# Kernel tuning notes

Hardware: AMD Instinct MI355X
Metric: run time of the kernel (lower is better)

## Reference

```python
import jax, jax.numpy as jnp
import numpy as np

IOU_THRESHOLD = 0.5


def setup_inputs() -> dict:
    key = jax.random.key(0)
    k_xy, k_wh, k_jit, k_cls, k_lab = jax.random.split(key, 5)
    B, P, T, C = 16, 16384, 128, 80
    # valid x1y1x2y2 ground-truth boxes in [0,1]
    xy = jax.random.uniform(k_xy, (B, T, 2), dtype=jnp.float32) * 0.7
    wh = jax.random.uniform(k_wh, (B, T, 2), dtype=jnp.float32) * 0.25 + 0.05
    true_bboxes = jnp.concatenate([xy, xy + wh], axis=-1)  # [B,T,4]
    # predictions: tiled GT boxes + small jitter so many pairs exceed IoU 0.5
    reps = P // T
    base = jnp.tile(true_bboxes, (1, reps, 1))  # [B,P,4]
    pred_bboxes = base + 0.02 * jax.random.normal(k_jit, (B, P, 4), dtype=jnp.float32)
    pred_classes = jax.random.normal(k_cls, (B, P, C), dtype=jnp.float32)
    true_labels = jax.random.randint(k_lab, (B, T), 0, C, dtype=jnp.int64)
    return {
        "pred_bboxes": pred_bboxes,
        "pred_classes": pred_classes,
        "true_bboxes": true_bboxes,
        "true_labels": true_labels,
    }


def _iou_matrix(pred, true):
    # pred [B,P,4], true [B,T,4] -> [B,P,T]
    p = pred[:, :, None, :]  # [B,P,1,4]
    t = true[:, None, :, :]  # [B,1,T,4]
    x1 = jnp.maximum(p[..., 0], t[..., 0])
    y1 = jnp.maximum(p[..., 1], t[..., 1])
    x2 = jnp.minimum(p[..., 2], t[..., 2])
    y2 = jnp.minimum(p[..., 3], t[..., 3])
    inter = jnp.clip(x2 - x1, 0.0) * jnp.clip(y2 - y1, 0.0)
    pa = (pred[..., 2] - pred[..., 0]) * (pred[..., 3] - pred[..., 1])  # [B,P]
    ta = (true[..., 2] - true[..., 0]) * (true[..., 3] - true[..., 1])  # [B,T]
    union = pa[:, :, None] + ta[:, None, :] - inter
    return inter / union


def _smooth_l1(d):
    ad = jnp.abs(d)
    return jnp.where(ad < 1.0, 0.5 * d * d, ad - 0.5)


def reference(pred_bboxes, pred_classes, true_bboxes, true_labels):
    B, P, _ = pred_bboxes.shape
    iou = _iou_matrix(pred_bboxes, true_bboxes)          # [B,P,T]
    max_iou = jnp.max(iou, axis=2)                       # [B,P]
    max_idx = jnp.argmax(iou, axis=2)                    # [B,P]
    matched_true = jnp.take_along_axis(
        true_bboxes, jnp.broadcast_to(max_idx[:, :, None], (B, P, 4)), axis=1
    )                                                    # [B,P,4]
    mask = (max_iou > IOU_THRESHOLD).astype(pred_bboxes.dtype)  # [B,P]
    elem = _smooth_l1(pred_bboxes - matched_true)        # [B,P,4]
    n_matched = jnp.sum(mask)
    bbox_loss = jnp.sum(elem * mask[:, :, None]) / jnp.maximum(4.0 * n_matched, 1.0)
    # classification: per image, first prediction's logits vs first GT label
    logits = pred_classes[:, 0, :]                       # [B,C]
    labels = true_labels[:, 0]                           # [B]
    logp = jax.nn.log_softmax(logits, axis=-1)
    cls_loss = -jnp.mean(jnp.take_along_axis(logp, labels[:, None], axis=1))
    return bbox_loss + cls_loss
```

## Files before the change

kernel.cpp:

```cpp
#include <hip/hip_runtime.h>
#include <hip/hip_bf16.h>
#include <math.h>

#define B_ 16
#define P_ 16384
#define T_ 128
#define C_ 80
#define IOU_THR 0.5f

__device__ __forceinline__ float smooth_l1(float d) {
    float ad = fabsf(d);
    return (ad < 1.0f) ? 0.5f * d * d : ad - 0.5f;
}

__global__ __launch_bounds__(256) void det_loss_main(
        const float* __restrict__ pred_bboxes,
        const float* __restrict__ true_bboxes,
        float* __restrict__ ws)
{
    const int blocks_per_b = P_ / 256;
    const int b    = blockIdx.x / blocks_per_b;
    const int pblk = blockIdx.x % blocks_per_b;
    const int tid  = threadIdx.x;

    __shared__ float4 tb[T_];
    if (tid < T_) {
        tb[tid] = ((const float4*)true_bboxes)[b * T_ + tid];
    }
    __syncthreads();

    const int p = pblk * 256 + tid;
    const float4 pb = ((const float4*)pred_bboxes)[(size_t)b * P_ + p];
    const float pa = (pb.z - pb.x) * (pb.w - pb.y);

    float best = -1.0f;
    int   bidx = 0;
    #pragma unroll 4
    for (int t = 0; t < T_; ++t) {
        const float4 t4 = tb[t];
        const float x1 = fmaxf(pb.x, t4.x);
        const float y1 = fmaxf(pb.y, t4.y);
        const float x2 = fminf(pb.z, t4.z);
        const float y2 = fminf(pb.w, t4.w);
        const float iw = fmaxf(x2 - x1, 0.0f);
        const float ih = fmaxf(y2 - y1, 0.0f);
        const float inter = iw * ih;
        const float ta = (t4.z - t4.x) * (t4.w - t4.y);
        const float iou = inter / (pa + ta - inter);
        if (iou > best) { best = iou; bidx = t; }
    }

    float contrib = 0.0f, cnt = 0.0f;
    if (best > IOU_THR) {
        const float4 t4 = tb[bidx];
        contrib = smooth_l1(pb.x - t4.x) + smooth_l1(pb.y - t4.y)
                + smooth_l1(pb.z - t4.z) + smooth_l1(pb.w - t4.w);
        cnt = 1.0f;
    }

    #pragma unroll
    for (int off = 32; off > 0; off >>= 1) {
        contrib += __shfl_down(contrib, off, 64);
        cnt     += __shfl_down(cnt,     off, 64);
    }
    __shared__ float sc[4], sn[4];
    const int wave = tid >> 6, lane = tid & 63;
    if (lane == 0) { sc[wave] = contrib; sn[wave] = cnt; }
    __syncthreads();
    if (tid == 0) {
        atomicAdd(&ws[0], sc[0] + sc[1] + sc[2] + sc[3]);
        atomicAdd(&ws[1], sn[0] + sn[1] + sn[2] + sn[3]);
    }
}

__global__ __launch_bounds__(64) void det_loss_final(
        const float* __restrict__ pred_classes,
        const int*   __restrict__ true_labels,
        const float* __restrict__ ws,
        float* __restrict__ out)
{
    const int tid = threadIdx.x;
    __shared__ float rowloss[B_];
    if (tid < B_) {
        const float* row = pred_classes + (size_t)tid * P_ * C_;
        const int lab = true_labels[tid * T_];
        float m = -INFINITY;
        for (int c = 0; c < C_; ++c) m = fmaxf(m, row[c]);
        float s = 0.0f;
        for (int c = 0; c < C_; ++c) s += expf(row[c] - m);
        rowloss[tid] = -(row[lab] - m - logf(s));
    }
    __syncthreads();
    if (tid == 0) {
        float cl = 0.0f;
        for (int b = 0; b < B_; ++b) cl += rowloss[b];
        cl *= (1.0f / B_);
        const float bbox = ws[0] / fmaxf(4.0f * ws[1], 1.0f);
        out[0] = bbox + cl;
    }
}

extern "C" void kernel_launch(void* const* d_in, const int* in_sizes, int n_in,
                              void* d_out, int out_size, void* d_ws, size_t ws_size,
                              hipStream_t stream) {
    const float* pred_bboxes  = (const float*)d_in[0];
    const float* pred_classes = (const float*)d_in[1];
    const float* true_bboxes  = (const float*)d_in[2];
    const int*   true_labels  = (const int*)d_in[3];
    float* out = (float*)d_out;
    float* ws  = (float*)d_ws;

    hipMemsetAsync(ws, 0, 2 * sizeof(float), stream);

    det_loss_main<<<B_ * (P_ / 256), 256, 0, stream>>>(pred_bboxes, true_bboxes, ws);
    det_loss_final<<<1, 64, 0, stream>>>(pred_classes, true_labels, ws, out);
}
```

Measured before the change: 158.2 us.

## Process two predictions per thread, use division-free IoU argmax, drop atomics and memset

Each thread now handles two prediction boxes, so every shared-memory load of a ground-truth box is reused twice. The IoU comparison is done by cross-multiplying intersection and union instead of dividing, and the threshold becomes 2*inter > union. Per-block partial sums go to a workspace array, which removes the atomics and the memset launch. The final kernel reduces those partials and computes log-softmax with wave shuffles. The cross-multiplied comparison can pick a different argmax from the reference when values tie or sit near rounding limits.

```diff
diff --git a/kernel.cpp b/kernel.cpp
--- a/kernel.cpp
+++ b/kernel.cpp
@@ -6,7 +6,7 @@
 #define P_ 16384
 #define T_ 128
 #define C_ 80
-#define IOU_THR 0.5f
+
 
 __device__ __forceinline__ float smooth_l1(float d) {
     float ad = fabsf(d);
@@ -18,44 +18,63 @@
         const float* __restrict__ true_bboxes,
         float* __restrict__ ws)
 {
-    const int blocks_per_b = P_ / 256;
+    const int blocks_per_b = P_ / 512;
     const int b    = blockIdx.x / blocks_per_b;
     const int pblk = blockIdx.x % blocks_per_b;
     const int tid  = threadIdx.x;
 
     __shared__ float4 tb[T_];
-    if (tid < T_) {
-        tb[tid] = ((const float4*)true_bboxes)[b * T_ + tid];
-    }
+    if (tid < T_) tb[tid] = ((const float4*)true_bboxes)[b * T_ + tid];
     __syncthreads();
 
-    const int p = pblk * 256 + tid;
-    const float4 pb = ((const float4*)pred_bboxes)[(size_t)b * P_ + p];
-    const float pa = (pb.z - pb.x) * (pb.w - pb.y);
+    const float4* pbase = (const float4*)pred_bboxes + (size_t)b * P_ + pblk * 512;
+    const float4 pA = pbase[tid];
+    const float4 pB = pbase[tid + 256];
+    const float paA = (pA.z - pA.x) * (pA.w - pA.y);
+    const float paB = (pB.z - pB.x) * (pB.w - pB.y);
 
-    float best = -1.0f;
-    int   bidx = 0;
-    #pragma unroll 4
+    float biA = 0.0f, buA = 1.0f; int bxA = 0;
+    float biB = 0.0f, buB = 1.0f; int bxB = 0;
+
+    #pragma unroll 8
     for (int t = 0; t < T_; ++t) {
         const float4 t4 = tb[t];
-        const float x1 = fmaxf(pb.x, t4.x);
-        const float y1 = fmaxf(pb.y, t4.y);
-        const float x2 = fminf(pb.z, t4.z);
-        const float y2 = fminf(pb.w, t4.w);
-        const float iw = fmaxf(x2 - x1, 0.0f);
-        const float ih = fmaxf(y2 - y1, 0.0f);
-        const float inter = iw * ih;
         const float ta = (t4.z - t4.x) * (t4.w - t4.y);
-        const float iou = inter / (pa + ta - inter);
-        if (iou > best) { best = iou; bidx = t; }
+
+        {
+            const float iw = fmaxf(fminf(pA.z, t4.z) - fmaxf(pA.x, t4.x), 0.0f);
+            const float ih = fmaxf(fminf(pA.w, t4.w) - fmaxf(pA.y, t4.y), 0.0f);
+            const float inter = iw * ih;
+            const float u = (paA + ta) - inter;
+            const bool upd = inter * buA > biA * u;
+            biA = upd ? inter : biA;
+            buA = upd ? u : buA;
+            bxA = upd ? t : bxA;
+        }
+        {
+            const float iw = fmaxf(fminf(pB.z, t4.z) - fmaxf(pB.x, t4.x), 0.0f);
+            const float ih = fmaxf(fminf(pB.w, t4.w) - fmaxf(pB.y, t4.y), 0.0f);
+            const float inter = iw * ih;
+            const float u = (paB + ta) - inter;
+            const bool upd = inter * buB > biB * u;
+            biB = upd ? inter : biB;
+            buB = upd ? u : buB;
+            bxB = upd ? t : bxB;
+        }
     }
 
     float contrib = 0.0f, cnt = 0.0f;
-    if (best > IOU_THR) {
-        const float4 t4 = tb[bidx];
-        contrib = smooth_l1(pb.x - t4.x) + smooth_l1(pb.y - t4.y)
-                + smooth_l1(pb.z - t4.z) + smooth_l1(pb.w - t4.w);
-        cnt = 1.0f;
+    if (2.0f * biA > buA) {
+        const float4 m4 = tb[bxA];
+        contrib += smooth_l1(pA.x - m4.x) + smooth_l1(pA.y - m4.y)
+                 + smooth_l1(pA.z - m4.z) + smooth_l1(pA.w - m4.w);
+        cnt += 1.0f;
+    }
+    if (2.0f * biB > buB) {
+        const float4 m4 = tb[bxB];
+        contrib += smooth_l1(pB.x - m4.x) + smooth_l1(pB.y - m4.y)
+                 + smooth_l1(pB.z - m4.z) + smooth_l1(pB.w - m4.w);
+        cnt += 1.0f;
     }
 
     #pragma unroll
@@ -68,35 +87,57 @@
     if (lane == 0) { sc[wave] = contrib; sn[wave] = cnt; }
     __syncthreads();
     if (tid == 0) {
-        atomicAdd(&ws[0], sc[0] + sc[1] + sc[2] + sc[3]);
-        atomicAdd(&ws[1], sn[0] + sn[1] + sn[2] + sn[3]);
+        ws[blockIdx.x]       = sc[0] + sc[1] + sc[2] + sc[3];
+        ws[512 + blockIdx.x] = sn[0] + sn[1] + sn[2] + sn[3];
     }
 }
 
-__global__ __launch_bounds__(64) void det_loss_final(
+__global__ __launch_bounds__(1024) void det_loss_final(
         const float* __restrict__ pred_classes,
         const int*   __restrict__ true_labels,
         const float* __restrict__ ws,
         float* __restrict__ out)
 {
     const int tid = threadIdx.x;
+    const int wave = tid >> 6, lane = tid & 63;
+
     __shared__ float rowloss[B_];
-    if (tid < B_) {
-        const float* row = pred_classes + (size_t)tid * P_ * C_;
-        const int lab = true_labels[tid * T_];
-        float m = -INFINITY;
-        for (int c = 0; c < C_; ++c) m = fmaxf(m, row[c]);
-        float s = 0.0f;
-        for (int c = 0; c < C_; ++c) s += expf(row[c] - m);
-        rowloss[tid] = -(row[lab] - m - logf(s));
+    __shared__ float wc[16], wn[16];
+
+    const float* row = pred_classes + (size_t)wave * P_ * C_;
+    const float v0 = row[lane];
+    const float v1 = (lane < C_ - 64) ? row[lane + 64] : -INFINITY;
+    float m = fmaxf(v0, v1);
+    #pragma unroll
+    for (int off = 32; off > 0; off >>= 1) m = fmaxf(m, __shfl_xor(m, off, 64));
+    float s = expf(v0 - m) + ((lane < C_ - 64) ? expf(v1 - m) : 0.0f);
+    #pragma unroll
+    for (int off = 32; off > 0; off >>= 1) s += __shfl_xor(s, off, 64);
+    if (lane == 0) {
+        const int lab = true_labels[wave * T_];
+        rowloss[wave] = -(row[lab] - m - logf(s));
     }
+
+    float sc = 0.0f, sn = 0.0f;
+    if (tid < 128) {
+        const float4 c4 = ((const float4*)ws)[tid];
+        const float4 n4 = ((const float4*)(ws + 512))[tid];
+        sc = c4.x + c4.y + c4.z + c4.w;
+        sn = n4.x + n4.y + n4.z + n4.w;
+    }
+    #pragma unroll
+    for (int off = 32; off > 0; off >>= 1) {
+        sc += __shfl_down(sc, off, 64);
+        sn += __shfl_down(sn, off, 64);
+    }
+    if (lane == 0) { wc[wave] = sc; wn[wave] = sn; }
     __syncthreads();
+
     if (tid == 0) {
-        float cl = 0.0f;
-        for (int b = 0; b < B_; ++b) cl += rowloss[b];
-        cl *= (1.0f / B_);
-        const float bbox = ws[0] / fmaxf(4.0f * ws[1], 1.0f);
-        out[0] = bbox + cl;
+        float C = 0.0f, N = 0.0f, cl = 0.0f;
+        #pragma unroll
+        for (int w = 0; w < 16; ++w) { C += wc[w]; N += wn[w]; cl += rowloss[w]; }
+        out[0] = C / fmaxf(4.0f * N, 1.0f) + cl * (1.0f / B_);
     }
 }
 
@@ -110,8 +151,6 @@
     float* out = (float*)d_out;
     float* ws  = (float*)d_ws;
 
-    hipMemsetAsync(ws, 0, 2 * sizeof(float), stream);
-
-    det_loss_main<<<B_ * (P_ / 256), 256, 0, stream>>>(pred_bboxes, true_bboxes, ws);
-    det_loss_final<<<1, 64, 0, stream>>>(pred_classes, true_labels, ws, out);
+    det_loss_main<<<B_ * (P_ / 512), 256, 0, stream>>>(pred_bboxes, true_bboxes, ws);
+    det_loss_final<<<1, 1024, 0, stream>>>(pred_classes, true_labels, ws, out);
 }
```

Result: faster. 133.5 us (-15.6%).
